# Kernel tuning notes

Measured on AMD Instinct MI355X. Metric: run time of the kernel, lower is better.

Reference implementation:

```python
import jax, jax.numpy as jnp
import numpy as np

COMMITMENT_COST = 0.25


def setup_inputs() -> dict:
    key = jax.random.key(0)
    k1, k2 = jax.random.split(key)
    x = jax.random.normal(k1, (32, 256, 32, 32), dtype=jnp.float32)
    codebook = jax.random.normal(k2, (1024, 256), dtype=jnp.float32) * 0.02
    return {"x": x, "codebook": codebook}


def reference(x, codebook):
    # x: [B, C, H, W] -> z: [B, H, W, C] (NHWC), C = embedding_dim
    B, C, H, W = x.shape
    z = jnp.transpose(x, (0, 2, 3, 1))
    zf = z.reshape(-1, C)  # [N, C], N = B*H*W
    # squared euclidean distance: ||z||^2 - 2 z.e + ||e||^2  -> [N, K]
    d = (
        jnp.sum(zf * zf, axis=-1, keepdims=True)
        - 2.0 * (zf @ codebook.T)
        + jnp.sum(codebook * codebook, axis=-1)
    )
    encoding_indices = jnp.argmin(d, axis=1)  # [N]
    quantized = codebook[encoding_indices].reshape(z.shape)  # [B, H, W, C]

    # training losses (entropy_loss_ratio == 0 -> entropy branch skipped)
    sg = jax.lax.stop_gradient
    e_latent_loss = jnp.mean((sg(quantized) - z) ** 2) * COMMITMENT_COST
    q_latent_loss = jnp.mean((quantized - sg(z)) ** 2)
    quantizer_loss = e_latent_loss + q_latent_loss

    # straight-through estimator
    quantized_st = z + sg(quantized - z)
    out = jnp.transpose(quantized_st, (0, 3, 1, 2))  # back to NCHW
    return out, quantizer_loss, e_latent_loss, q_latent_loss, encoding_indices
```

## Files before the change

kernel.cpp:

```cpp
#include <hip/hip_runtime.h>
#include <cfloat>

#define C_DIM   256
#define HW      1024
#define N_ROWS  32768
#define K_CODES 1024
#define ROWS    64
#define NCHUNK  32
#define WCHUNK_BYTES 8192
#define LISTCAP 128
#define DELTA   0.008f
#define CMASK   0xFFFFFFE0u
#define ZSTRIDE 260

#define OUT_ELEMS 8388608
#define LOSS_OFF  8388608
#define IDX_OFF   8388611

typedef _Float16 half8 __attribute__((ext_vector_type(8)));
typedef _Float16 f16x4 __attribute__((ext_vector_type(4)));
typedef float    f32x4 __attribute__((ext_vector_type(4)));

#define AS1 __attribute__((address_space(1)))
#define AS3 __attribute__((address_space(3)))

#define OFF_EBUF  0
#define OFF_EN    66560
#define OFF_S32   70656
#define OFF_M1W   70912
#define OFF_THR   71424
#define OFF_RES   71680
#define OFF_FIDX  72192
#define OFF_LCNT  72448
#define OFF_LMETA 72704
#define SMEM_BYTES 74752

#define QT_STRIDE 258

#define DPP_MIN(x, ctrl) fminf((x), __int_as_float(__builtin_amdgcn_update_dpp(0, __float_as_int(x), (ctrl), 0xf, 0xf, true)))

__global__ void prep_kernel(const float* __restrict__ cb, float* __restrict__ enorm,
                            char* __restrict__ cb16) {
    int k = blockIdx.x * 4 + (threadIdx.x >> 6);
    int lane = threadIdx.x & 63;
    int c0 = lane * 4;
    float4 v = *(const float4*)(cb + k * C_DIM + c0);
    double s = (double)v.x * v.x + (double)v.y * v.y + (double)v.z * v.z + (double)v.w * v.w;
    #pragma unroll
    for (int m = 1; m < 64; m <<= 1) s += __shfl_xor(s, m, 64);
    if (lane == 0) enorm[k] = (float)s;
    f16x4 h;
    h[0] = (_Float16)v.x; h[1] = (_Float16)v.y; h[2] = (_Float16)v.z; h[3] = (_Float16)v.w;
    int dst = ((k >> 4) << 13) + ((c0 >> 5) << 10) + (((c0 >> 3) & 3) << 8)
            + ((k & 15) << 4) + ((c0 & 7) << 1);
    *(f16x4*)(cb16 + dst) = h;
}

__global__ __launch_bounds__(256, 2) void vq_main(
    const float* __restrict__ x, const float* __restrict__ cb,
    const float* __restrict__ enorm_g, const char* __restrict__ cb16,
    float* __restrict__ out, float* __restrict__ idx_out, float* __restrict__ t2_out)
{
    extern __shared__ char smem[];
    float* zt      = (float*)(smem + OFF_EBUF);
    float* qt      = (float*)(smem + OFF_EBUF);
    float* en_lds  = (float*)(smem + OFF_EN);
    float* S32     = (float*)(smem + OFF_S32);
    float* m1w     = (float*)(smem + OFF_M1W);
    float* thr     = (float*)(smem + OFF_THR);
    unsigned long long* res = (unsigned long long*)(smem + OFF_RES);
    int*   fidx    = (int*)(smem + OFF_FIDX);
    int*   lcnt    = (int*)(smem + OFF_LCNT);
    unsigned int* lmeta = (unsigned int*)(smem + OFF_LMETA);

    const int t    = threadIdx.x;
    const int lane = t & 63;
    const int wv   = t >> 6;
    const int wr   = wv >> 1;
    const int wc   = wv & 1;
    const int l15  = lane & 15;
    const int l4   = lane >> 4;
    const int row0 = blockIdx.x * ROWS;
    const int b    = row0 >> 10;
    const int hw0  = row0 & 1023;
    const float* xb = x + b * (C_DIM * HW) + hw0;

    char* ebw = smem + OFF_EBUF + wv * (2 * WCHUNK_BYTES);
    const char* cbw = cb16 + wc * WCHUNK_BYTES;

    {
        int g   = t & 15;
        int cb4 = t >> 4;
        for (int cc = cb4 * 4; cc < C_DIM; cc += 64) {
            float4 v0 = *(const float4*)(xb + (cc + 0) * HW + g * 4);
            float4 v1 = *(const float4*)(xb + (cc + 1) * HW + g * 4);
            float4 v2 = *(const float4*)(xb + (cc + 2) * HW + g * 4);
            float4 v3 = *(const float4*)(xb + (cc + 3) * HW + g * 4);
            *(float4*)&zt[(g * 4 + 0) * ZSTRIDE + cc] = make_float4(v0.x, v1.x, v2.x, v3.x);
            *(float4*)&zt[(g * 4 + 1) * ZSTRIDE + cc] = make_float4(v0.y, v1.y, v2.y, v3.y);
            *(float4*)&zt[(g * 4 + 2) * ZSTRIDE + cc] = make_float4(v0.z, v1.z, v2.z, v3.z);
            *(float4*)&zt[(g * 4 + 3) * ZSTRIDE + cc] = make_float4(v0.w, v1.w, v2.w, v3.w);
        }
        *(float4*)&en_lds[t * 4] = *(const float4*)(enorm_g + t * 4);
        if (t < 4) lcnt[t] = 0;
    }
    __syncthreads();

    {
        int r = t >> 2, seg = t & 3;
        const float* zr = &zt[r * ZSTRIDE + seg * 64];
        double s = 0.0;
        for (int c = 0; c < 64; c += 4) {
            float4 v = *(const float4*)(zr + c);
            s = fma((double)v.x, (double)v.x, s);
            s = fma((double)v.y, (double)v.y, s);
            s = fma((double)v.z, (double)v.z, s);
            s = fma((double)v.w, (double)v.w, s);
        }
        s += __shfl_xor(s, 1, 64);
        s += __shfl_xor(s, 2, 64);
        if (seg == 0) S32[r] = (float)s;
    }

    half8 af[2][8];
    #pragma unroll
    for (int rt = 0; rt < 2; rt++) {
        int row = wr * 32 + rt * 16 + l15;
        #pragma unroll
        for (int kk = 0; kk < 8; kk++) {
            int c0 = kk * 32 + l4 * 8;
            float4 a  = *(const float4*)&zt[row * ZSTRIDE + c0];
            float4 a2 = *(const float4*)&zt[row * ZSTRIDE + c0 + 4];
            half8 h;
            h[0] = (_Float16)(-2.0f * a.x);  h[1] = (_Float16)(-2.0f * a.y);
            h[2] = (_Float16)(-2.0f * a.z);  h[3] = (_Float16)(-2.0f * a.w);
            h[4] = (_Float16)(-2.0f * a2.x); h[5] = (_Float16)(-2.0f * a2.y);
            h[6] = (_Float16)(-2.0f * a2.z); h[7] = (_Float16)(-2.0f * a2.w);
            af[rt][kk] = h;
        }
    }
    __syncthreads();

    #pragma unroll
    for (int c2 = 0; c2 < 2; c2++) {
        const char* src = cbw + (c2 << 14);
        char* dst = ebw + c2 * WCHUNK_BYTES;
        #pragma unroll
        for (int i = 0; i < 8; i++) {
            __builtin_amdgcn_global_load_lds((const AS1 unsigned int*)(src + i * 1024 + lane * 16),
                                             (AS3 unsigned int*)(dst + i * 1024), 16, 0, 0);
        }
    }

    const int bbase  = (l4 << 8) + (l15 << 4);
    const int enbase = wc * 16 + l15;

    float u1[2][4], u2[2][4];
    #pragma unroll
    for (int rt = 0; rt < 2; rt++)
        #pragma unroll
        for (int r2 = 0; r2 < 4; r2++) { u1[rt][r2] = FLT_MAX; u2[rt][r2] = FLT_MAX; }

    for (int ch = 0; ch < NCHUNK; ch++) {
        if (ch == NCHUNK - 1) { asm volatile("s_waitcnt vmcnt(0)" ::: "memory"); }
        else                  { asm volatile("s_waitcnt vmcnt(8)" ::: "memory"); }
        __builtin_amdgcn_sched_barrier(0);

        const char* ebc = ebw + (ch & 1) * WCHUNK_BYTES;
        half8 bf[8];
        #pragma unroll
        for (int kk = 0; kk < 8; kk++)
            bf[kk] = *(const half8*)(ebc + bbase + (kk << 10));
        asm volatile("s_waitcnt lgkmcnt(0)" ::: "memory");
        __builtin_amdgcn_sched_barrier(0);

        if (ch + 2 < NCHUNK) {
            const char* src = cbw + ((ch + 2) << 14);
            char* dst = ebw + (ch & 1) * WCHUNK_BYTES;
            #pragma unroll
            for (int i = 0; i < 8; i++) {
                __builtin_amdgcn_global_load_lds((const AS1 unsigned int*)(src + i * 1024 + lane * 16),
                                                 (AS3 unsigned int*)(dst + i * 1024), 16, 0, 0);
            }
        }

        const float en = en_lds[enbase + ch * 32];
        f32x4 acc0 = {en, en, en, en};
        f32x4 acc1 = {en, en, en, en};
        #pragma unroll
        for (int kk = 0; kk < 8; kk++) {
            acc0 = __builtin_amdgcn_mfma_f32_16x16x32_f16(af[0][kk], bf[kk], acc0, 0, 0, 0);
            acc1 = __builtin_amdgcn_mfma_f32_16x16x32_f16(af[1][kk], bf[kk], acc1, 0, 0, 0);
        }
        #pragma unroll
        for (int r2 = 0; r2 < 4; r2++) {
            float a0 = __uint_as_float((__float_as_uint(acc0[r2]) & CMASK) | (unsigned)ch);
            u2[0][r2] = __builtin_amdgcn_fmed3f(a0, u1[0][r2], u2[0][r2]);
            u1[0][r2] = fminf(u1[0][r2], a0);
            float a1 = __uint_as_float((__float_as_uint(acc1[r2]) & CMASK) | (unsigned)ch);
            u2[1][r2] = __builtin_amdgcn_fmed3f(a1, u1[1][r2], u2[1][r2]);
            u1[1][r2] = fminf(u1[1][r2], a1);
        }
    }

    #pragma unroll
    for (int rt = 0; rt < 2; rt++) {
        #pragma unroll
        for (int r2 = 0; r2 < 4; r2++) {
            float m = u1[rt][r2];
            m = DPP_MIN(m, 0xB1);
            m = DPP_MIN(m, 0x4E);
            m = DPP_MIN(m, 0x141);
            m = DPP_MIN(m, 0x140);
            if (l15 == 0) m1w[wc * 64 + wr * 32 + rt * 16 + l4 * 4 + r2] = m;
        }
    }
    __syncthreads();
    if (t < 64) {
        thr[t] = fminf(m1w[t], m1w[64 + t]) + DELTA;
        res[t] = ~0ull;
    }
    __syncthreads();

    #pragma unroll
    for (int rt = 0; rt < 2; rt++) {
        #pragma unroll
        for (int r2 = 0; r2 < 4; r2++) {
            int row_l = wr * 32 + rt * 16 + l4 * 4 + r2;
            float tr = thr[row_l];
            if (u1[rt][r2] < tr) {
                int ch1 = (int)(__float_as_uint(u1[rt][r2]) & 31u);
                int code = ch1 * 32 + wc * 16 + l15;
                int slot = atomicAdd(&lcnt[wv], 1);
                if (slot < LISTCAP)
                    lmeta[wv * LISTCAP + slot] = ((unsigned)row_l << 16) | (unsigned)code;
            }
            if (u2[rt][r2] < tr) {
                int ch2 = (int)(__float_as_uint(u2[rt][r2]) & 31u);
                int code = ch2 * 32 + wc * 16 + l15;
                int slot = atomicAdd(&lcnt[wv], 1);
                if (slot < LISTCAP)
                    lmeta[wv * LISTCAP + slot] = ((unsigned)row_l << 16) | (unsigned)code;
            }
        }
    }
    __syncthreads();

    {
        int n = lcnt[wv]; if (n > LISTCAP) n = LISTCAP;
        for (int base = 0; base < n; base += 4) {
            int it = base + l4;
            if (it < n) {
                unsigned meta = lmeta[wv * LISTCAP + it];
                int row  = (int)(meta >> 16);
                int code = (int)(meta & 1023u);
                const float* xr = xb + row;
                const float* er = cb + code * C_DIM;
                double acc = 0.0;
                #pragma unroll
                for (int s2 = 0; s2 < 16; s2++) {
                    int c = l15 + 16 * s2;
                    acc = fma((double)xr[(size_t)c * HW], (double)er[c], acc);
                }
                acc += __shfl_xor(acc, 1, 64);
                acc += __shfl_xor(acc, 2, 64);
                acc += __shfl_xor(acc, 4, 64);
                acc += __shfl_xor(acc, 8, 64);
                if (l15 == 0) {
                    float Mf = (float)acc;
                    float t2 = __fadd_rn(__fsub_rn(S32[row], __fmul_rn(2.0f, Mf)), en_lds[code]);
                    unsigned long long pk =
                        ((unsigned long long)__float_as_uint(t2) << 32) | (unsigned long long)(unsigned)code;
                    atomicMin(&res[row], pk);
                }
            }
        }
    }
    __syncthreads();

    if (t < 64) {
        unsigned long long v = res[t];
        int code = (int)(v & 1023u);
        fidx[t] = code;
        idx_out[row0 + t] = (float)code;
        t2_out[row0 + t] = __uint_as_float((unsigned)(v >> 32));
    }

    float* ob = out + b * (C_DIM * HW) + hw0;
    #pragma unroll
    for (int half = 0; half < 2; half++) {
        __syncthreads();
        for (int idx = t; idx < 32 * 64; idx += 256) {
            int r  = idx >> 6;
            int c4 = idx & 63;
            const float* er = cb + fidx[half * 32 + r] * C_DIM;
            *(float4*)&qt[r * QT_STRIDE + c4 * 4] = *(const float4*)(er + c4 * 4);
        }
        __syncthreads();
        int rr = t & 31;
        int cg = t >> 5;
        for (int cc = cg; cc < C_DIM; cc += 8) {
            ob[cc * HW + half * 32 + rr] = qt[rr * QT_STRIDE + cc];
        }
    }
}

__global__ void loss_kernel(const float* __restrict__ t2min, float* __restrict__ losses) {
    __shared__ double sh[256];
    int t = threadIdx.x;
    double a = 0.0;
    const int per = N_ROWS / 256;
    for (int i = t * per; i < t * per + per; i++) a += (double)t2min[i];
    sh[t] = a;
    __syncthreads();
    for (int s = 128; s > 0; s >>= 1) {
        if (t < s) sh[t] += sh[t + s];
        __syncthreads();
    }
    if (t == 0) {
        double M = sh[0] / (double)OUT_ELEMS;
        losses[0] = (float)(1.25 * M);
        losses[1] = (float)(0.25 * M);
        losses[2] = (float)(M);
    }
}

extern "C" void kernel_launch(void* const* d_in, const int* in_sizes, int n_in,
                              void* d_out, int out_size, void* d_ws, size_t ws_size,
                              hipStream_t stream) {
    const float* x  = (const float*)d_in[0];
    const float* cb = (const float*)d_in[1];
    float* out     = (float*)d_out;
    float* losses  = out + LOSS_OFF;
    float* idx_out = out + IDX_OFF;

    char*  cb16     = (char*)d_ws;
    float* t2ws     = (float*)((char*)d_ws + 524288);
    float* enorm_ws = (float*)((char*)d_ws + 524288 + 131072);

    hipFuncSetAttribute(reinterpret_cast<const void*>(vq_main),
                        hipFuncAttributeMaxDynamicSharedMemorySize, SMEM_BYTES);

    prep_kernel<<<K_CODES / 4, 256, 0, stream>>>(cb, enorm_ws, cb16);
    vq_main<<<N_ROWS / ROWS, 256, SMEM_BYTES, stream>>>(x, cb, enorm_ws, cb16, out, idx_out, t2ws);
    loss_kernel<<<1, 256, 0, stream>>>(t2ws, losses);
}
```

Measured before the change: 69.00 us.

## Share codebook chunks across all waves via block-wide double-buffered LDS superchunks

Each wave previously streamed its own private copy of the fp16 codebook into LDS with per-wave double buffering, so waves that share a codebook column fetched the same data twice. Now all four waves cooperatively load one 32KB superchunk covering two 32-code chunks into a shared double buffer, and a block-wide barrier guards each superchunk. This halves codebook global traffic per block and lets each wave process two chunks per iteration. The cost is a full s_waitcnt vmcnt(0) plus an s_barrier every superchunk, which couples the waves and shrinks the prefetch depth.

```diff
diff --git a/kernel.cpp b/kernel.cpp
--- a/kernel.cpp
+++ b/kernel.cpp
@@ -6,8 +6,8 @@
 #define N_ROWS  32768
 #define K_CODES 1024
 #define ROWS    64
-#define NCHUNK  32
-#define WCHUNK_BYTES 8192
+#define NSUPER  16
+#define SUPER_BYTES 32768
 #define LISTCAP 128
 #define DELTA   0.008f
 #define CMASK   0xFFFFFFE0u
@@ -64,6 +64,7 @@
     extern __shared__ char smem[];
     float* zt      = (float*)(smem + OFF_EBUF);
     float* qt      = (float*)(smem + OFF_EBUF);
+    char*  ebuf    = smem + OFF_EBUF;
     float* en_lds  = (float*)(smem + OFF_EN);
     float* S32     = (float*)(smem + OFF_S32);
     float* m1w     = (float*)(smem + OFF_M1W);
@@ -85,8 +86,7 @@
     const int hw0  = row0 & 1023;
     const float* xb = x + b * (C_DIM * HW) + hw0;
 
-    char* ebw = smem + OFF_EBUF + wv * (2 * WCHUNK_BYTES);
-    const char* cbw = cb16 + wc * WCHUNK_BYTES;
+    const int qofs = wv * 8192;
 
     {
         int g   = t & 15;
@@ -142,17 +142,12 @@
     __syncthreads();
 
     #pragma unroll
-    for (int c2 = 0; c2 < 2; c2++) {
-        const char* src = cbw + (c2 << 14);
-        char* dst = ebw + c2 * WCHUNK_BYTES;
-        #pragma unroll
-        for (int i = 0; i < 8; i++) {
-            __builtin_amdgcn_global_load_lds((const AS1 unsigned int*)(src + i * 1024 + lane * 16),
-                                             (AS3 unsigned int*)(dst + i * 1024), 16, 0, 0);
-        }
-    }
-
-    const int bbase  = (l4 << 8) + (l15 << 4);
+    for (int i = 0; i < 8; i++) {
+        __builtin_amdgcn_global_load_lds((const AS1 unsigned int*)(cb16 + qofs + i * 1024 + lane * 16),
+                                         (AS3 unsigned int*)(ebuf + qofs + i * 1024), 16, 0, 0);
+    }
+
+    const int bbase  = (wc << 13) + (l4 << 8) + (l15 << 4);
     const int enbase = wc * 16 + l15;
 
     float u1[2][4], u2[2][4];
@@ -161,22 +156,17 @@
         #pragma unroll
         for (int r2 = 0; r2 < 4; r2++) { u1[rt][r2] = FLT_MAX; u2[rt][r2] = FLT_MAX; }
 
-    for (int ch = 0; ch < NCHUNK; ch++) {
-        if (ch == NCHUNK - 1) { asm volatile("s_waitcnt vmcnt(0)" ::: "memory"); }
-        else                  { asm volatile("s_waitcnt vmcnt(8)" ::: "memory"); }
+    for (int sc = 0; sc < NSUPER; sc++) {
+        asm volatile("s_waitcnt vmcnt(0)" ::: "memory");
         __builtin_amdgcn_sched_barrier(0);
-
-        const char* ebc = ebw + (ch & 1) * WCHUNK_BYTES;
-        half8 bf[8];
-        #pragma unroll
-        for (int kk = 0; kk < 8; kk++)
-            bf[kk] = *(const half8*)(ebc + bbase + (kk << 10));
-        asm volatile("s_waitcnt lgkmcnt(0)" ::: "memory");
+        __builtin_amdgcn_s_barrier();
         __builtin_amdgcn_sched_barrier(0);
 
-        if (ch + 2 < NCHUNK) {
-            const char* src = cbw + ((ch + 2) << 14);
-            char* dst = ebw + (ch & 1) * WCHUNK_BYTES;
+        const char* ebc = ebuf + (sc & 1) * SUPER_BYTES;
+
+        if (sc + 1 < NSUPER) {
+            const char* src = cb16 + (sc + 1) * SUPER_BYTES + qofs;
+            char* dst = ebuf + ((sc + 1) & 1) * SUPER_BYTES + qofs;
             #pragma unroll
             for (int i = 0; i < 8; i++) {
                 __builtin_amdgcn_global_load_lds((const AS1 unsigned int*)(src + i * 1024 + lane * 16),
@@ -184,22 +174,53 @@
             }
         }
 
-        const float en = en_lds[enbase + ch * 32];
-        f32x4 acc0 = {en, en, en, en};
-        f32x4 acc1 = {en, en, en, en};
-        #pragma unroll
-        for (int kk = 0; kk < 8; kk++) {
-            acc0 = __builtin_amdgcn_mfma_f32_16x16x32_f16(af[0][kk], bf[kk], acc0, 0, 0, 0);
-            acc1 = __builtin_amdgcn_mfma_f32_16x16x32_f16(af[1][kk], bf[kk], acc1, 0, 0, 0);
-        }
-        #pragma unroll
-        for (int r2 = 0; r2 < 4; r2++) {
-            float a0 = __uint_as_float((__float_as_uint(acc0[r2]) & CMASK) | (unsigned)ch);
-            u2[0][r2] = __builtin_amdgcn_fmed3f(a0, u1[0][r2], u2[0][r2]);
-            u1[0][r2] = fminf(u1[0][r2], a0);
-            float a1 = __uint_as_float((__float_as_uint(acc1[r2]) & CMASK) | (unsigned)ch);
-            u2[1][r2] = __builtin_amdgcn_fmed3f(a1, u1[1][r2], u2[1][r2]);
-            u1[1][r2] = fminf(u1[1][r2], a1);
+        {
+            const int ch = 2 * sc;
+            half8 bf[8];
+            #pragma unroll
+            for (int kk = 0; kk < 8; kk++)
+                bf[kk] = *(const half8*)(ebc + bbase + (kk << 10));
+            const float en = en_lds[enbase + ch * 32];
+            f32x4 acc0 = {en, en, en, en};
+            f32x4 acc1 = {en, en, en, en};
+            #pragma unroll
+            for (int kk = 0; kk < 8; kk++) {
+                acc0 = __builtin_amdgcn_mfma_f32_16x16x32_f16(af[0][kk], bf[kk], acc0, 0, 0, 0);
+                acc1 = __builtin_amdgcn_mfma_f32_16x16x32_f16(af[1][kk], bf[kk], acc1, 0, 0, 0);
+            }
+            #pragma unroll
+            for (int r2 = 0; r2 < 4; r2++) {
+                float a0 = __uint_as_float((__float_as_uint(acc0[r2]) & CMASK) | (unsigned)ch);
+                u2[0][r2] = __builtin_amdgcn_fmed3f(a0, u1[0][r2], u2[0][r2]);
+                u1[0][r2] = fminf(u1[0][r2], a0);
+                float a1 = __uint_as_float((__float_as_uint(acc1[r2]) & CMASK) | (unsigned)ch);
+                u2[1][r2] = __builtin_amdgcn_fmed3f(a1, u1[1][r2], u2[1][r2]);
+                u1[1][r2] = fminf(u1[1][r2], a1);
+            }
+        }
+        {
+            const int ch = 2 * sc + 1;
+            half8 bf[8];
+            #pragma unroll
+            for (int kk = 0; kk < 8; kk++)
+                bf[kk] = *(const half8*)(ebc + 16384 + bbase + (kk << 10));
+            const float en = en_lds[enbase + ch * 32];
+            f32x4 acc0 = {en, en, en, en};
+            f32x4 acc1 = {en, en, en, en};
+            #pragma unroll
+            for (int kk = 0; kk < 8; kk++) {
+                acc0 = __builtin_amdgcn_mfma_f32_16x16x32_f16(af[0][kk], bf[kk], acc0, 0, 0, 0);
+                acc1 = __builtin_amdgcn_mfma_f32_16x16x32_f16(af[1][kk], bf[kk], acc1, 0, 0, 0);
+            }
+            #pragma unroll
+            for (int r2 = 0; r2 < 4; r2++) {
+                float a0 = __uint_as_float((__float_as_uint(acc0[r2]) & CMASK) | (unsigned)ch);
+                u2[0][r2] = __builtin_amdgcn_fmed3f(a0, u1[0][r2], u2[0][r2]);
+                u1[0][r2] = fminf(u1[0][r2], a0);
+                float a1 = __uint_as_float((__float_as_uint(acc1[r2]) & CMASK) | (unsigned)ch);
+                u2[1][r2] = __builtin_amdgcn_fmed3f(a1, u1[1][r2], u2[1][r2]);
+                u1[1][r2] = fminf(u1[1][r2], a1);
+            }
         }
     }
 
```

Measured after the change: 66.00 us. 1.05x faster.
